# Performance work log

Measured on AMD Instinct MI355X. Metric: run time of the kernel, lower is better.

The kernel has to match this reference:

```python
import jax, jax.numpy as jnp
import numpy as np
from jax import lax

TAU = 10.0
THR = 1.0
ALPHA = float(np.exp(-1.0 / TAU))  # leak factor exp(-dt/tau), dt=1


def conv2d(x, w, pad):
    # x: [N,C,H,W], w: [O,I,kh,kw]
    return lax.conv_general_dilated(
        x, w, window_strides=(1, 1), padding=[(pad, pad), (pad, pad)],
        dimension_numbers=('NCHW', 'OIHW', 'NCHW'))


def avgpool(x, k):
    n, c, h, w = x.shape
    return x.reshape(n, c, h // k, k, w // k, k).mean(axis=(3, 5))


def exp_leak(x):
    # x: [T, ...]; v[t] = alpha*v[t-1] + x[t]; outputs membrane each step
    def step(v, xt):
        v = ALPHA * v + xt
        return v, v
    _, y = lax.scan(step, jnp.zeros_like(x[0]), x)
    return y


def lif(x):
    # LIF with SingleSpike + MembraneSubtract reset (norm_input=False)
    def step(v, xt):
        v = ALPHA * v + xt
        s = (v >= THR).astype(v.dtype)
        return v - s * THR, s
    _, s = lax.scan(step, jnp.zeros_like(x[0]), x)
    return s


def forward(x, conv1_w, conv2_w, lin_w):
    B, T = x.shape[:2]
    h = avgpool(conv2d(x.reshape(B * T, 2, 32, 32), conv1_w, 2), 4)  # [BT,4,8,8]
    h = h.reshape(B, T, 4, 8, 8).swapaxes(0, 1)                       # [T,B,4,8,8]
    h = lif(exp_leak(h)).swapaxes(0, 1).reshape(B * T, 4, 8, 8)
    h = avgpool(conv2d(h, conv2_w, 1), 2)                             # [BT,8,4,4]
    h = h.reshape(B, T, 8, 4, 4).swapaxes(0, 1)                       # [T,B,8,4,4]
    h = lif(exp_leak(h)).swapaxes(0, 1).reshape(B, T, 8 * 4 * 4)      # [B,T,128]
    return jnp.einsum('btf,of->bto', h, lin_w)                        # [B,T,2]


def setup_inputs() -> dict:
    key = jax.random.key(0)
    k1, k2, k3, k4 = jax.random.split(key, 4)
    B, T = 128, 100
    x = jax.random.uniform(k1, (B, T, 2, 32, 32), dtype=jnp.float32)
    conv1_w = jax.random.normal(k2, (4, 2, 5, 5), dtype=jnp.float32) / np.sqrt(2 * 5 * 5)
    conv2_w = jax.random.normal(k3, (8, 4, 3, 3), dtype=jnp.float32) / np.sqrt(4 * 3 * 3)
    lin_w = jax.random.normal(k4, (2, 128), dtype=jnp.float32) / np.sqrt(128)
    return {'x': x, 'conv1_w': conv1_w, 'conv2_w': conv2_w, 'lin_w': lin_w}


def reference(x, conv1_w, conv2_w, lin_w):
    return forward(x, conv1_w, conv2_w, lin_w)
```

## Files before the change

kernel.cpp:

```cpp
#include <hip/hip_runtime.h>

#define ALPHA 0.90483741803595957f

__global__ void prep_weights(const float* __restrict__ w1, const float* __restrict__ w2,
                             float* __restrict__ w1e, float* __restrict__ w2e) {
    int idx = blockIdx.x * 256 + threadIdx.x;
    if (idx < 512) {
        int v = idx & 7, u = (idx >> 3) & 7, ch = (idx >> 6) & 1, oc = idx >> 7;
        float s = 0.f;
        for (int a = 0; a < 5; ++a) {
            int i = u - a; if (i < 0 || i > 3) continue;
            for (int b = 0; b < 5; ++b) {
                int j = v - b; if (j < 0 || j > 3) continue;
                s += w1[((oc * 2 + ch) * 5 + a) * 5 + b];
            }
        }
        w1e[idx] = s * (1.f / 16.f);
    } else if (idx < 1024) {
        int k = idx - 512;
        int v = k & 3, u = (k >> 2) & 3, ch = (k >> 4) & 3, oc = k >> 6;
        float s = 0.f;
        for (int a = 0; a < 3; ++a) {
            int i = u - a; if (i < 0 || i > 1) continue;
            for (int b = 0; b < 3; ++b) {
                int j = v - b; if (j < 0 || j > 1) continue;
                s += w2[((oc * 4 + ch) * 3 + a) * 3 + b];
            }
        }
        w2e[k] = s * 0.25f;
    }
}

__global__ __launch_bounds__(256) void conv1_pool(const float* __restrict__ x,
                                                  const float* __restrict__ w1e,
                                                  float* __restrict__ y1) {
    __shared__ __align__(16) float tile[4][2][36][36];
    int tid = threadIdx.x;

    float4* t4 = (float4*)&tile[0][0][0][0];
    #pragma unroll
    for (int k = 0; k < 11; ++k) {
        int i = tid + k * 256;
        if (i < 2592) t4[i] = make_float4(0.f, 0.f, 0.f, 0.f);
    }
    __syncthreads();

    int li = tid >> 6, pos = tid & 63;
    long gi = (long)blockIdx.x * 4 + li;
    const float* src = x + gi * 2048;
    #pragma unroll
    for (int k = 0; k < 8; ++k) {
        int e = k * 256 + pos * 4;
        float4 d = *(const float4*)(src + e);
        int ch = e >> 10, rem = e & 1023, r = rem >> 5, c = rem & 31;
        float* dst = &tile[li][ch][r + 2][c + 2];
        dst[0] = d.x; dst[1] = d.y; dst[2] = d.z; dst[3] = d.w;
    }
    __syncthreads();

    int p = pos >> 3, q = pos & 7;
    float acc0 = 0.f, acc1 = 0.f, acc2 = 0.f, acc3 = 0.f;
    #pragma unroll
    for (int ch = 0; ch < 2; ++ch) {
        #pragma unroll
        for (int r = 0; r < 8; ++r) {
            const float* row = &tile[li][ch][4 * p + r][4 * q];
            float4 a = *(const float4*)row;
            float4 b = *(const float4*)(row + 4);
            float in[8] = {a.x, a.y, a.z, a.w, b.x, b.y, b.z, b.w};
            #pragma unroll
            for (int c = 0; c < 8; ++c) {
                float xi = in[c];
                acc0 += w1e[((0 * 2 + ch) * 8 + r) * 8 + c] * xi;
                acc1 += w1e[((1 * 2 + ch) * 8 + r) * 8 + c] * xi;
                acc2 += w1e[((2 * 2 + ch) * 8 + r) * 8 + c] * xi;
                acc3 += w1e[((3 * 2 + ch) * 8 + r) * 8 + c] * xi;
            }
        }
    }
    float* dst = y1 + gi * 256 + pos;
    dst[0] = acc0; dst[64] = acc1; dst[128] = acc2; dst[192] = acc3;
}

__global__ __launch_bounds__(64, 1) void fused_wave(const float* __restrict__ y1,
                                                    const float* __restrict__ w2e,
                                                    float* __restrict__ s2g) {
    __shared__ float tile[808];
    int lane = threadIdx.x;
    int b = blockIdx.x;

    #pragma unroll
    for (int k = 0; k < 13; ++k) {
        int i = lane + k * 64;
        if (i < 808) tile[i] = 0.f;
    }

    int r1 = lane >> 3, c1 = lane & 7;
    int posq = (r1 + 1) * 10 + (c1 + 1);
    float* wrA = &tile[posq * 4];
    float* wrB = &tile[404 + posq * 4];

    int oc = lane >> 4, p = (lane >> 2) & 3, q = lane & 3;

    float wa[64], wb[64];
    #pragma unroll
    for (int k = 0; k < 16; ++k) {
        float4 ta = *(const float4*)(w2e + oc * 64 + k * 4);
        float4 tb = *(const float4*)(w2e + (oc + 4) * 64 + k * 4);
        wa[k * 4 + 0] = ta.x; wa[k * 4 + 1] = ta.y; wa[k * 4 + 2] = ta.z; wa[k * 4 + 3] = ta.w;
        wb[k * 4 + 0] = tb.x; wb[k * 4 + 1] = tb.y; wb[k * 4 + 2] = tb.z; wb[k * 4 + 3] = tb.w;
    }

    const float* rbase = &tile[((2 * p) * 10 + 2 * q) * 4];
    if (p & 1) rbase += 404;

    const float* src = y1 + (long)b * 25600 + lane;
    float* dst = s2g + (long)b * 100 * 128 + lane;

    float cur0 = src[0], cur1 = src[64], cur2 = src[128], cur3 = src[192];
    float v10 = 0.f, v20 = 0.f, v11 = 0.f, v21 = 0.f;
    float v12 = 0.f, v22 = 0.f, v13 = 0.f, v23 = 0.f;
    float w1a = 0.f, w2a = 0.f, w1b = 0.f, w2b = 0.f;

    __syncthreads();

    for (int t = 0; t < 100; ++t) {
        const float* nsrc = src + (t < 99 ? (t + 1) * 256 : 0);
        float n0 = nsrc[0], n1 = nsrc[64], n2 = nsrc[128], n3 = nsrc[192];

        v10 = ALPHA * v10 + cur0; v20 = ALPHA * v20 + v10;
        float s0 = (v20 >= 1.f) ? 1.f : 0.f; v20 -= s0;
        v11 = ALPHA * v11 + cur1; v21 = ALPHA * v21 + v11;
        float s1 = (v21 >= 1.f) ? 1.f : 0.f; v21 -= s1;
        v12 = ALPHA * v12 + cur2; v22 = ALPHA * v22 + v12;
        float s2 = (v22 >= 1.f) ? 1.f : 0.f; v22 -= s2;
        v13 = ALPHA * v13 + cur3; v23 = ALPHA * v23 + v13;
        float s3 = (v23 >= 1.f) ? 1.f : 0.f; v23 -= s3;

        float4 sp = make_float4(s0, s1, s2, s3);
        *(float4*)wrA = sp;
        *(float4*)wrB = sp;
        __syncthreads();

        float qv[64];
        #pragma unroll
        for (int rr = 0; rr < 4; ++rr) {
            #pragma unroll
            for (int cc = 0; cc < 4; ++cc) {
                float4 tq = *(const float4*)(rbase + rr * 40 + cc * 4);
                int o = (rr * 4 + cc) * 4;
                qv[o + 0] = tq.x; qv[o + 1] = tq.y; qv[o + 2] = tq.z; qv[o + 3] = tq.w;
            }
        }

        float acca = 0.f, accb = 0.f;
        #pragma unroll
        for (int ch = 0; ch < 4; ++ch)
            #pragma unroll
            for (int rr = 0; rr < 4; ++rr)
                #pragma unroll
                for (int cc = 0; cc < 4; ++cc) {
                    float xv = qv[(rr * 4 + cc) * 4 + ch];
                    acca += wa[ch * 16 + rr * 4 + cc] * xv;
                    accb += wb[ch * 16 + rr * 4 + cc] * xv;
                }

        w1a = ALPHA * w1a + acca; w2a = ALPHA * w2a + w1a;
        float sa = (w2a >= 1.f) ? 1.f : 0.f; w2a -= sa;
        w1b = ALPHA * w1b + accb; w2b = ALPHA * w2b + w1b;
        float sb = (w2b >= 1.f) ? 1.f : 0.f; w2b -= sb;

        dst[t * 128] = sa;
        dst[t * 128 + 64] = sb;

        __syncthreads();
        cur0 = n0; cur1 = n1; cur2 = n2; cur3 = n3;
    }
}

__global__ __launch_bounds__(256) void linear_out(const float* __restrict__ s2,
                                                  const float* __restrict__ lw,
                                                  float* __restrict__ out) {
    int tid = threadIdx.x;
    long bt = (long)blockIdx.x * 4 + (tid >> 6);
    int lane = tid & 63;
    float2 v = *(const float2*)(s2 + bt * 128 + lane * 2);
    float w00 = lw[lane * 2], w01 = lw[lane * 2 + 1];
    float w10 = lw[128 + lane * 2], w11 = lw[128 + lane * 2 + 1];
    float a0 = v.x * w00 + v.y * w01;
    float a1 = v.x * w10 + v.y * w11;
    #pragma unroll
    for (int off = 32; off; off >>= 1) {
        a0 += __shfl_down(a0, off);
        a1 += __shfl_down(a1, off);
    }
    if (lane == 0) { out[bt * 2] = a0; out[bt * 2 + 1] = a1; }
}

extern "C" void kernel_launch(void* const* d_in, const int* in_sizes, int n_in,
                              void* d_out, int out_size, void* d_ws, size_t ws_size,
                              hipStream_t stream) {
    const float* x  = (const float*)d_in[0];
    const float* w1 = (const float*)d_in[1];
    const float* w2 = (const float*)d_in[2];
    const float* lw = (const float*)d_in[3];
    float* out = (float*)d_out;

    float* ws   = (float*)d_ws;
    float* w1e  = ws;
    float* w2e  = ws + 512;
    float* y1   = ws + 1024;
    float* s2g  = y1 + 3276800;

    prep_weights<<<4, 256, 0, stream>>>(w1, w2, w1e, w2e);
    conv1_pool<<<3200, 256, 0, stream>>>(x, w1e, y1);
    fused_wave<<<128, 64, 0, stream>>>(y1, w2e, s2g);
    linear_out<<<3200, 256, 0, stream>>>(s2g, lw, out);
}
```

Measured before the change: 215.9 us.

## Fuse linear readout into recurrent wave kernel with double-buffered LDS, no barriers

The final linear projection now runs inside the single-wavefront recurrent kernel as a cross-lane reduction, so the intermediate spike tensor is no longer written to global memory and the separate linear kernel launch is gone. The time loop is unrolled by two, using separate even/odd LDS tiles. Because each block is exactly one wavefront, the __syncthreads barriers are dropped. Input prefetch moves two steps ahead. In exchange, each step adds a chain of shuffle reductions on the serial critical path. The barrier-free LDS handoff relies on a 64-thread block executing as a single wave.

```diff
diff --git a/kernel.cpp b/kernel.cpp
--- a/kernel.cpp
+++ b/kernel.cpp
@@ -84,21 +84,25 @@
 
 __global__ __launch_bounds__(64, 1) void fused_wave(const float* __restrict__ y1,
                                                     const float* __restrict__ w2e,
-                                                    float* __restrict__ s2g) {
-    __shared__ float tile[808];
+                                                    const float* __restrict__ lw,
+                                                    float* __restrict__ out) {
+    __shared__ float tEv[808];
+    __shared__ float tOd[808];
     int lane = threadIdx.x;
     int b = blockIdx.x;
 
     #pragma unroll
     for (int k = 0; k < 13; ++k) {
         int i = lane + k * 64;
-        if (i < 808) tile[i] = 0.f;
+        if (i < 808) { tEv[i] = 0.f; tOd[i] = 0.f; }
     }
 
     int r1 = lane >> 3, c1 = lane & 7;
-    int posq = (r1 + 1) * 10 + (c1 + 1);
-    float* wrA = &tile[posq * 4];
-    float* wrB = &tile[404 + posq * 4];
+    int posq = ((r1 + 1) * 10 + (c1 + 1)) * 4;
+    float* wrE0 = &tEv[posq];
+    float* wrE1 = &tEv[404 + posq];
+    float* wrO0 = &tOd[posq];
+    float* wrO1 = &tOd[404 + posq];
 
     int oc = lane >> 4, p = (lane >> 2) & 3, q = lane & 3;
 
@@ -111,90 +115,128 @@
         wb[k * 4 + 0] = tb.x; wb[k * 4 + 1] = tb.y; wb[k * 4 + 2] = tb.z; wb[k * 4 + 3] = tb.w;
     }
 
-    const float* rbase = &tile[((2 * p) * 10 + 2 * q) * 4];
-    if (p & 1) rbase += 404;
+    int rbq = ((2 * p) * 10 + 2 * q) * 4 + ((p & 1) ? 404 : 0);
+    const float* rbE = &tEv[rbq];
+    const float* rbO = &tOd[rbq];
+
+    float lw0a = lw[lane],       lw0b = lw[lane + 64];
+    float lw1a = lw[lane + 128], lw1b = lw[lane + 192];
 
     const float* src = y1 + (long)b * 25600 + lane;
-    float* dst = s2g + (long)b * 100 * 128 + lane;
-
-    float cur0 = src[0], cur1 = src[64], cur2 = src[128], cur3 = src[192];
+    float* outp = out + (long)b * 200;
+
+    float cur0 = src[0],   cur1 = src[64],  cur2 = src[128], cur3 = src[192];
+    float nx0  = src[256], nx1  = src[320], nx2  = src[384], nx3  = src[448];
     float v10 = 0.f, v20 = 0.f, v11 = 0.f, v21 = 0.f;
     float v12 = 0.f, v22 = 0.f, v13 = 0.f, v23 = 0.f;
     float w1a = 0.f, w2a = 0.f, w1b = 0.f, w2b = 0.f;
 
-    __syncthreads();
-
-    for (int t = 0; t < 100; ++t) {
-        const float* nsrc = src + (t < 99 ? (t + 1) * 256 : 0);
-        float n0 = nsrc[0], n1 = nsrc[64], n2 = nsrc[128], n3 = nsrc[192];
+    for (int tt = 0; tt < 50; ++tt) {
+        int tA = 2 * tt;
+        const float* nsA = src + (tA + 2 < 100 ? (tA + 2) * 256 : 0);
+        float pA0 = nsA[0], pA1 = nsA[64], pA2 = nsA[128], pA3 = nsA[192];
 
         v10 = ALPHA * v10 + cur0; v20 = ALPHA * v20 + v10;
-        float s0 = (v20 >= 1.f) ? 1.f : 0.f; v20 -= s0;
+        float sA0 = (v20 >= 1.f) ? 1.f : 0.f; v20 -= sA0;
         v11 = ALPHA * v11 + cur1; v21 = ALPHA * v21 + v11;
-        float s1 = (v21 >= 1.f) ? 1.f : 0.f; v21 -= s1;
+        float sA1 = (v21 >= 1.f) ? 1.f : 0.f; v21 -= sA1;
         v12 = ALPHA * v12 + cur2; v22 = ALPHA * v22 + v12;
-        float s2 = (v22 >= 1.f) ? 1.f : 0.f; v22 -= s2;
+        float sA2 = (v22 >= 1.f) ? 1.f : 0.f; v22 -= sA2;
         v13 = ALPHA * v13 + cur3; v23 = ALPHA * v23 + v13;
-        float s3 = (v23 >= 1.f) ? 1.f : 0.f; v23 -= s3;
-
-        float4 sp = make_float4(s0, s1, s2, s3);
-        *(float4*)wrA = sp;
-        *(float4*)wrB = sp;
-        __syncthreads();
-
-        float qv[64];
+        float sA3 = (v23 >= 1.f) ? 1.f : 0.f; v23 -= sA3;
+
+        float4 spA = make_float4(sA0, sA1, sA2, sA3);
+        *(float4*)wrE0 = spA;
+        *(float4*)wrE1 = spA;
+
+        float qa[64];
         #pragma unroll
         for (int rr = 0; rr < 4; ++rr) {
             #pragma unroll
             for (int cc = 0; cc < 4; ++cc) {
-                float4 tq = *(const float4*)(rbase + rr * 40 + cc * 4);
+                float4 tq = *(const float4*)(rbE + rr * 40 + cc * 4);
                 int o = (rr * 4 + cc) * 4;
-                qv[o + 0] = tq.x; qv[o + 1] = tq.y; qv[o + 2] = tq.z; qv[o + 3] = tq.w;
-            }
-        }
-
-        float acca = 0.f, accb = 0.f;
+                qa[o + 0] = tq.x; qa[o + 1] = tq.y; qa[o + 2] = tq.z; qa[o + 3] = tq.w;
+            }
+        }
+        float accaA = 0.f, accbA = 0.f;
         #pragma unroll
         for (int ch = 0; ch < 4; ++ch)
             #pragma unroll
             for (int rr = 0; rr < 4; ++rr)
                 #pragma unroll
                 for (int cc = 0; cc < 4; ++cc) {
-                    float xv = qv[(rr * 4 + cc) * 4 + ch];
-                    acca += wa[ch * 16 + rr * 4 + cc] * xv;
-                    accb += wb[ch * 16 + rr * 4 + cc] * xv;
+                    float xv = qa[(rr * 4 + cc) * 4 + ch];
+                    accaA += wa[ch * 16 + rr * 4 + cc] * xv;
+                    accbA += wb[ch * 16 + rr * 4 + cc] * xv;
                 }
-
-        w1a = ALPHA * w1a + acca; w2a = ALPHA * w2a + w1a;
-        float sa = (w2a >= 1.f) ? 1.f : 0.f; w2a -= sa;
-        w1b = ALPHA * w1b + accb; w2b = ALPHA * w2b + w1b;
-        float sb = (w2b >= 1.f) ? 1.f : 0.f; w2b -= sb;
-
-        dst[t * 128] = sa;
-        dst[t * 128 + 64] = sb;
-
-        __syncthreads();
-        cur0 = n0; cur1 = n1; cur2 = n2; cur3 = n3;
-    }
-}
-
-__global__ __launch_bounds__(256) void linear_out(const float* __restrict__ s2,
-                                                  const float* __restrict__ lw,
-                                                  float* __restrict__ out) {
-    int tid = threadIdx.x;
-    long bt = (long)blockIdx.x * 4 + (tid >> 6);
-    int lane = tid & 63;
-    float2 v = *(const float2*)(s2 + bt * 128 + lane * 2);
-    float w00 = lw[lane * 2], w01 = lw[lane * 2 + 1];
-    float w10 = lw[128 + lane * 2], w11 = lw[128 + lane * 2 + 1];
-    float a0 = v.x * w00 + v.y * w01;
-    float a1 = v.x * w10 + v.y * w11;
-    #pragma unroll
-    for (int off = 32; off; off >>= 1) {
-        a0 += __shfl_down(a0, off);
-        a1 += __shfl_down(a1, off);
-    }
-    if (lane == 0) { out[bt * 2] = a0; out[bt * 2 + 1] = a1; }
+        w1a = ALPHA * w1a + accaA; w2a = ALPHA * w2a + w1a;
+        float saA = (w2a >= 1.f) ? 1.f : 0.f; w2a -= saA;
+        w1b = ALPHA * w1b + accbA; w2b = ALPHA * w2b + w1b;
+        float sbA = (w2b >= 1.f) ? 1.f : 0.f; w2b -= sbA;
+
+        int tB = tA + 1;
+        const float* nsB = src + (tB + 2 < 100 ? (tB + 2) * 256 : 0);
+        float pB0 = nsB[0], pB1 = nsB[64], pB2 = nsB[128], pB3 = nsB[192];
+
+        v10 = ALPHA * v10 + nx0; v20 = ALPHA * v20 + v10;
+        float sB0 = (v20 >= 1.f) ? 1.f : 0.f; v20 -= sB0;
+        v11 = ALPHA * v11 + nx1; v21 = ALPHA * v21 + v11;
+        float sB1 = (v21 >= 1.f) ? 1.f : 0.f; v21 -= sB1;
+        v12 = ALPHA * v12 + nx2; v22 = ALPHA * v22 + v12;
+        float sB2 = (v22 >= 1.f) ? 1.f : 0.f; v22 -= sB2;
+        v13 = ALPHA * v13 + nx3; v23 = ALPHA * v23 + v13;
+        float sB3 = (v23 >= 1.f) ? 1.f : 0.f; v23 -= sB3;
+
+        float4 spB = make_float4(sB0, sB1, sB2, sB3);
+        *(float4*)wrO0 = spB;
+        *(float4*)wrO1 = spB;
+
+        float qb[64];
+        #pragma unroll
+        for (int rr = 0; rr < 4; ++rr) {
+            #pragma unroll
+            for (int cc = 0; cc < 4; ++cc) {
+                float4 tq = *(const float4*)(rbO + rr * 40 + cc * 4);
+                int o = (rr * 4 + cc) * 4;
+                qb[o + 0] = tq.x; qb[o + 1] = tq.y; qb[o + 2] = tq.z; qb[o + 3] = tq.w;
+            }
+        }
+        float accaB = 0.f, accbB = 0.f;
+        #pragma unroll
+        for (int ch = 0; ch < 4; ++ch)
+            #pragma unroll
+            for (int rr = 0; rr < 4; ++rr)
+                #pragma unroll
+                for (int cc = 0; cc < 4; ++cc) {
+                    float xv = qb[(rr * 4 + cc) * 4 + ch];
+                    accaB += wa[ch * 16 + rr * 4 + cc] * xv;
+                    accbB += wb[ch * 16 + rr * 4 + cc] * xv;
+                }
+        w1a = ALPHA * w1a + accaB; w2a = ALPHA * w2a + w1a;
+        float saB = (w2a >= 1.f) ? 1.f : 0.f; w2a -= saB;
+        w1b = ALPHA * w1b + accbB; w2b = ALPHA * w2b + w1b;
+        float sbB = (w2b >= 1.f) ? 1.f : 0.f; w2b -= sbB;
+
+        float a0 = saA * lw0a + sbA * lw0b;
+        float a1 = saA * lw1a + sbA * lw1b;
+        float b0 = saB * lw0a + sbB * lw0b;
+        float b1 = saB * lw1a + sbB * lw1b;
+        #pragma unroll
+        for (int off = 32; off; off >>= 1) {
+            a0 += __shfl_xor(a0, off);
+            a1 += __shfl_xor(a1, off);
+            b0 += __shfl_xor(b0, off);
+            b1 += __shfl_xor(b1, off);
+        }
+        if (lane == 0) {
+            *(float2*)(outp + tA * 2) = make_float2(a0, a1);
+            *(float2*)(outp + tB * 2) = make_float2(b0, b1);
+        }
+
+        cur0 = pA0; cur1 = pA1; cur2 = pA2; cur3 = pA3;
+        nx0 = pB0; nx1 = pB1; nx2 = pB2; nx3 = pB3;
+    }
 }
 
 extern "C" void kernel_launch(void* const* d_in, const int* in_sizes, int n_in,
@@ -210,10 +252,8 @@
     float* w1e  = ws;
     float* w2e  = ws + 512;
     float* y1   = ws + 1024;
-    float* s2g  = y1 + 3276800;
 
     prep_weights<<<4, 256, 0, stream>>>(w1, w2, w1e, w2e);
     conv1_pool<<<3200, 256, 0, stream>>>(x, w1e, y1);
-    fused_wave<<<128, 64, 0, stream>>>(y1, w2e, s2g);
-    linear_out<<<3200, 256, 0, stream>>>(s2g, lw, out);
-}
+    fused_wave<<<128, 64, 0, stream>>>(y1, w2e, lw, out);
+}
```

Result: no change. 212.2 us (-1.7%).

## Double-buffer LDS spike tiles and drop per-step barriers in fused_wave

Applied to the files above, without the earlier changes.

Splits the shared spike tile into even and odd buffers and software-pipelines the time loop two steps at a time, so the layer-1 LIF and LDS write for step t+1 overlap with the conv2 and LIF for step t. The __syncthreads calls are removed, which relies on the block being a single 64-lane wavefront. Global loads are prefetched several timesteps ahead, and empty asm statements pin the weights in VGPRs. The cost is higher register pressure from two 64-float q arrays plus the weights, with some risk of spilling.

```diff
diff --git a/kernel.cpp b/kernel.cpp
--- a/kernel.cpp
+++ b/kernel.cpp
@@ -82,23 +82,78 @@
     dst[0] = acc0; dst[64] = acc1; dst[128] = acc2; dst[192] = acc3;
 }
 
+#define READW(base, Q)                                                        \
+    {                                                                         \
+        _Pragma("unroll")                                                     \
+        for (int rr = 0; rr < 4; ++rr) {                                      \
+            _Pragma("unroll")                                                 \
+            for (int cc = 0; cc < 4; ++cc) {                                  \
+                float4 tq = *(const float4*)((base) + rr * 40 + cc * 4);      \
+                int o = (rr * 4 + cc) * 4;                                    \
+                Q[o + 0] = tq.x; Q[o + 1] = tq.y;                             \
+                Q[o + 2] = tq.z; Q[o + 3] = tq.w;                             \
+            }                                                                 \
+        }                                                                     \
+    }
+
+#define SCAN1_WRITE(in0, in1, in2, in3, d0, d1)                               \
+    {                                                                         \
+        v10 = ALPHA * v10 + (in0); v20 = ALPHA * v20 + v10;                   \
+        float s0 = (v20 >= 1.f) ? 1.f : 0.f; v20 -= s0;                       \
+        v11 = ALPHA * v11 + (in1); v21 = ALPHA * v21 + v11;                   \
+        float s1 = (v21 >= 1.f) ? 1.f : 0.f; v21 -= s1;                       \
+        v12 = ALPHA * v12 + (in2); v22 = ALPHA * v22 + v12;                   \
+        float s2 = (v22 >= 1.f) ? 1.f : 0.f; v22 -= s2;                       \
+        v13 = ALPHA * v13 + (in3); v23 = ALPHA * v23 + v13;                   \
+        float s3 = (v23 >= 1.f) ? 1.f : 0.f; v23 -= s3;                       \
+        float4 sp = make_float4(s0, s1, s2, s3);                              \
+        *(float4*)(d0) = sp;                                                  \
+        *(float4*)(d1) = sp;                                                  \
+    }
+
+#define CONV_SCAN2_STORE(Q, t)                                                \
+    {                                                                         \
+        float acca = 0.f, accb = 0.f;                                         \
+        _Pragma("unroll")                                                     \
+        for (int ch = 0; ch < 4; ++ch) {                                      \
+            _Pragma("unroll")                                                 \
+            for (int rr = 0; rr < 4; ++rr) {                                  \
+                _Pragma("unroll")                                             \
+                for (int cc = 0; cc < 4; ++cc) {                              \
+                    float xv = Q[(rr * 4 + cc) * 4 + ch];                     \
+                    acca += wa[ch * 16 + rr * 4 + cc] * xv;                   \
+                    accb += wb[ch * 16 + rr * 4 + cc] * xv;                   \
+                }                                                             \
+            }                                                                 \
+        }                                                                     \
+        w1a = ALPHA * w1a + acca; w2a = ALPHA * w2a + w1a;                    \
+        float sa = (w2a >= 1.f) ? 1.f : 0.f; w2a -= sa;                       \
+        w1b = ALPHA * w1b + accb; w2b = ALPHA * w2b + w1b;                    \
+        float sb = (w2b >= 1.f) ? 1.f : 0.f; w2b -= sb;                       \
+        dst[(t) * 128]      = sa;                                             \
+        dst[(t) * 128 + 64] = sb;                                             \
+    }
+
 __global__ __launch_bounds__(64, 1) void fused_wave(const float* __restrict__ y1,
                                                     const float* __restrict__ w2e,
                                                     float* __restrict__ s2g) {
-    __shared__ float tile[808];
+    __shared__ float tE[808];
+    __shared__ float tO[808];
     int lane = threadIdx.x;
     int b = blockIdx.x;
 
     #pragma unroll
     for (int k = 0; k < 13; ++k) {
         int i = lane + k * 64;
-        if (i < 808) tile[i] = 0.f;
+        if (i < 808) { tE[i] = 0.f; tO[i] = 0.f; }
     }
 
     int r1 = lane >> 3, c1 = lane & 7;
-    int posq = (r1 + 1) * 10 + (c1 + 1);
-    float* wrA = &tile[posq * 4];
-    float* wrB = &tile[404 + posq * 4];
+    int posq = ((r1 + 1) * 10 + (c1 + 1)) * 4;
+    float* wE0 = &tE[posq];
+    float* wE1 = &tE[404 + posq];
+    float* wO0 = &tO[posq];
+    float* wO1 = &tO[404 + posq];
 
     int oc = lane >> 4, p = (lane >> 2) & 3, q = lane & 3;
 
@@ -111,71 +166,58 @@
         wb[k * 4 + 0] = tb.x; wb[k * 4 + 1] = tb.y; wb[k * 4 + 2] = tb.z; wb[k * 4 + 3] = tb.w;
     }
 
-    const float* rbase = &tile[((2 * p) * 10 + 2 * q) * 4];
-    if (p & 1) rbase += 404;
+    int rbq = ((2 * p) * 10 + 2 * q) * 4 + ((p & 1) ? 404 : 0);
+    const float* rbE = &tE[rbq];
+    const float* rbO = &tO[rbq];
+
+    #pragma unroll
+    for (int k = 0; k < 64; ++k) {
+        asm volatile("" : "+v"(wa[k]));
+        asm volatile("" : "+v"(wb[k]));
+    }
 
     const float* src = y1 + (long)b * 25600 + lane;
-    float* dst = s2g + (long)b * 100 * 128 + lane;
-
-    float cur0 = src[0], cur1 = src[64], cur2 = src[128], cur3 = src[192];
+    float* dst = s2g + (long)b * 12800 + lane;
+
+    float x0  = src[0],    x1  = src[64],   x2  = src[128],  x3  = src[192];
+    float c10 = src[256],  c11 = src[320],  c12 = src[384],  c13 = src[448];
+    float c20 = src[512],  c21 = src[576],  c22 = src[640],  c23 = src[704];
+    float p10 = src[768],  p11 = src[832],  p12 = src[896],  p13 = src[960];
+    float p20 = src[1024], p21 = src[1088], p22 = src[1152], p23 = src[1216];
+
     float v10 = 0.f, v20 = 0.f, v11 = 0.f, v21 = 0.f;
     float v12 = 0.f, v22 = 0.f, v13 = 0.f, v23 = 0.f;
     float w1a = 0.f, w2a = 0.f, w1b = 0.f, w2b = 0.f;
 
-    __syncthreads();
-
-    for (int t = 0; t < 100; ++t) {
-        const float* nsrc = src + (t < 99 ? (t + 1) * 256 : 0);
-        float n0 = nsrc[0], n1 = nsrc[64], n2 = nsrc[128], n3 = nsrc[192];
-
-        v10 = ALPHA * v10 + cur0; v20 = ALPHA * v20 + v10;
-        float s0 = (v20 >= 1.f) ? 1.f : 0.f; v20 -= s0;
-        v11 = ALPHA * v11 + cur1; v21 = ALPHA * v21 + v11;
-        float s1 = (v21 >= 1.f) ? 1.f : 0.f; v21 -= s1;
-        v12 = ALPHA * v12 + cur2; v22 = ALPHA * v22 + v12;
-        float s2 = (v22 >= 1.f) ? 1.f : 0.f; v22 -= s2;
-        v13 = ALPHA * v13 + cur3; v23 = ALPHA * v23 + v13;
-        float s3 = (v23 >= 1.f) ? 1.f : 0.f; v23 -= s3;
-
-        float4 sp = make_float4(s0, s1, s2, s3);
-        *(float4*)wrA = sp;
-        *(float4*)wrB = sp;
-        __syncthreads();
-
-        float qv[64];
-        #pragma unroll
-        for (int rr = 0; rr < 4; ++rr) {
-            #pragma unroll
-            for (int cc = 0; cc < 4; ++cc) {
-                float4 tq = *(const float4*)(rbase + rr * 40 + cc * 4);
-                int o = (rr * 4 + cc) * 4;
-                qv[o + 0] = tq.x; qv[o + 1] = tq.y; qv[o + 2] = tq.z; qv[o + 3] = tq.w;
-            }
-        }
-
-        float acca = 0.f, accb = 0.f;
-        #pragma unroll
-        for (int ch = 0; ch < 4; ++ch)
-            #pragma unroll
-            for (int rr = 0; rr < 4; ++rr)
-                #pragma unroll
-                for (int cc = 0; cc < 4; ++cc) {
-                    float xv = qv[(rr * 4 + cc) * 4 + ch];
-                    acca += wa[ch * 16 + rr * 4 + cc] * xv;
-                    accb += wb[ch * 16 + rr * 4 + cc] * xv;
-                }
-
-        w1a = ALPHA * w1a + acca; w2a = ALPHA * w2a + w1a;
-        float sa = (w2a >= 1.f) ? 1.f : 0.f; w2a -= sa;
-        w1b = ALPHA * w1b + accb; w2b = ALPHA * w2b + w1b;
-        float sb = (w2b >= 1.f) ? 1.f : 0.f; w2b -= sb;
-
-        dst[t * 128] = sa;
-        dst[t * 128 + 64] = sb;
-
-        __syncthreads();
-        cur0 = n0; cur1 = n1; cur2 = n2; cur3 = n3;
-    }
+    float qa[64], qb[64];
+
+    SCAN1_WRITE(x0, x1, x2, x3, wE0, wE1)
+    READW(rbE, qa)
+
+    for (int i = 0; i < 49; ++i) {
+        int t5 = 2 * i + 5, t6 = 2 * i + 6;
+        const float* a5 = src + (t5 < 100 ? t5 * 256 : 0);
+        const float* a6 = src + (t6 < 100 ? t6 * 256 : 0);
+        float n10 = a5[0], n11 = a5[64], n12 = a5[128], n13 = a5[192];
+        float n20 = a6[0], n21 = a6[64], n22 = a6[128], n23 = a6[192];
+
+        SCAN1_WRITE(c10, c11, c12, c13, wO0, wO1)
+        READW(rbO, qb)
+        CONV_SCAN2_STORE(qa, 2 * i)
+        SCAN1_WRITE(c20, c21, c22, c23, wE0, wE1)
+        READW(rbE, qa)
+        CONV_SCAN2_STORE(qb, 2 * i + 1)
+
+        c10 = p10; c11 = p11; c12 = p12; c13 = p13;
+        c20 = p20; c21 = p21; c22 = p22; c23 = p23;
+        p10 = n10; p11 = n11; p12 = n12; p13 = n13;
+        p20 = n20; p21 = n21; p22 = n22; p23 = n23;
+    }
+
+    SCAN1_WRITE(c10, c11, c12, c13, wO0, wO1)
+    READW(rbO, qb)
+    CONV_SCAN2_STORE(qa, 98)
+    CONV_SCAN2_STORE(qb, 99)
 }
 
 __global__ __launch_bounds__(256) void linear_out(const float* __restrict__ s2,
```

Measured after the change: 204.2 us. 5.4% less time.
